# Performance work log

Hardware: AMD Instinct MI355X
Metric: run time of the kernel (lower is better)

The kernel has to match this reference:

```python
import jax, jax.numpy as jnp
import numpy as np

N_HEAD = 16
N_FEAT = 1024
D_K = N_FEAT // N_HEAD


def setup_inputs() -> dict:
    key = jax.random.key(0)
    ks = jax.random.split(key, 12)
    B, T, F = 4, 2048, N_FEAT
    s = 1.0 / np.sqrt(F)
    return {
        "query": jax.random.normal(ks[0], (B, T, F), dtype=jnp.float32),
        "key": jax.random.normal(ks[1], (B, T, F), dtype=jnp.float32),
        "value": jax.random.normal(ks[2], (B, T, F), dtype=jnp.float32),
        "mask": jnp.ones((B, 1, T), dtype=jnp.int32),
        "Wq": jax.random.normal(ks[3], (F, F), dtype=jnp.float32) * s,
        "bq": jax.random.normal(ks[4], (F,), dtype=jnp.float32) * 0.01,
        "Wk": jax.random.normal(ks[5], (F, F), dtype=jnp.float32) * s,
        "bk": jax.random.normal(ks[6], (F,), dtype=jnp.float32) * 0.01,
        "Wv": jax.random.normal(ks[7], (F, F), dtype=jnp.float32) * s,
        "bv": jax.random.normal(ks[8], (F,), dtype=jnp.float32) * 0.01,
        "Wo": jax.random.normal(ks[9], (F, F), dtype=jnp.float32) * s,
        "bo": jax.random.normal(ks[10], (F,), dtype=jnp.float32) * 0.01,
    }


def reference(query, key, value, mask, Wq, bq, Wk, bk, Wv, bv, Wo, bo):
    B, Tq, F = query.shape
    Tk = key.shape[1]
    h, dk = N_HEAD, D_K
    # torch nn.Linear: y = x @ W.T + b ; then view [B,T,h,dk] and transpose to [B,h,T,dk]
    q = (query @ Wq.T + bq).reshape(B, Tq, h, dk).transpose(0, 2, 1, 3)
    k = (key @ Wk.T + bk).reshape(B, Tk, h, dk).transpose(0, 2, 1, 3)
    v = (value @ Wv.T + bv).reshape(B, Tk, h, dk).transpose(0, 2, 1, 3)
    scale = 1.0 / np.sqrt(dk).astype(np.float32)
    scores = jnp.einsum("bhqd,bhkd->bhqk", q, k) * scale  # [B,h,Tq,Tk]
    # mask [B,1,Tk] -> unsqueeze(1) -> [B,1,1,Tk], True where mask == 0 (padded)
    pad = (mask[:, None, :, :] == 0)
    min_value = jnp.finfo(scores.dtype).min
    scores = jnp.where(pad, min_value, scores)
    atten = jax.nn.softmax(scores, axis=-1)
    atten = jnp.where(pad, 0.0, atten)
    # dropout_rate = 0.0 (eval): identity
    x = jnp.einsum("bhqk,bhkd->bhqd", atten, v)  # [B,h,Tq,dk]
    x = x.transpose(0, 2, 1, 3).reshape(B, Tq, h * dk)
    return x @ Wo.T + bo
```

## Files before the change

kernel.cpp:

```cpp
#include <hip/hip_runtime.h>
#include <hip/hip_bf16.h>


typedef unsigned short u16;
typedef unsigned long long u64;
typedef __attribute__((ext_vector_type(8))) short short8;
typedef __attribute__((ext_vector_type(4))) float f32x4;
typedef __attribute__((ext_vector_type(16))) float f32x16;
typedef __attribute__((ext_vector_type(4))) unsigned int u32x4;

#define GLOAD16(g, l) __builtin_amdgcn_global_load_lds( \
    (const __attribute__((address_space(1))) unsigned int*)(g), \
    (__attribute__((address_space(3))) unsigned int*)(l), 16, 0, 0)

__device__ __forceinline__ u16 f2bf(float x) {
  unsigned int u = __float_as_uint(x);
  return (u16)((u + 0x7fffu + ((u >> 16) & 1u)) >> 16);
}

__device__ __forceinline__ float fexp2(float x) {
#if __has_builtin(__builtin_amdgcn_exp2f)
  return __builtin_amdgcn_exp2f(x);
#else
  return exp2f(x);
#endif
}

__device__ __forceinline__ unsigned cvtpk(float lo, float hi) {
  unsigned r;
  asm("v_cvt_pk_bf16_f32 %0, %1, %2" : "=v"(r) : "v"(lo), "v"(hi));
  return r;
}

struct CvtArgs {
  const float* src[4];
  u16* dst[4];
};

__global__ __launch_bounds__(256) void cvt_multi(CvtArgs a, int shift) {
  const int id = blockIdx.x * 256 + threadIdx.x;
  const int seg = id >> shift;
  const int off = id & ((1 << shift) - 1);
  float4 v = ((const float4*)a.src[seg])[off];
  ushort4 o;
  o.x = f2bf(v.x); o.y = f2bf(v.y); o.z = f2bf(v.z); o.w = f2bf(v.w);
  ((ushort4*)a.dst[seg])[off] = o;
}

template <int EPI>
__global__ __launch_bounds__(256) void gemm_bt(const u16* __restrict__ A,
                                               const u16* __restrict__ Bw,
                                               const float* __restrict__ bias,
                                               void* __restrict__ Cout,
                                               float scale) {
  __shared__ u16 As[128 * 64];
  __shared__ u16 Bs[128 * 64];
  const int t = threadIdx.x;
  const int lane = t & 63;
  const int w = t >> 6;
  const int wm = w >> 1, wn = w & 1;
  const int l15 = lane & 15, l4 = lane >> 4;

  const int bid = blockIdx.x;
  const int swz = (bid & 7) * 64 + (bid >> 3);
  const int brow = swz >> 3;
  const int bcol = swz & 7;

  f32x4 acc[4][4] = {};

  const int srow = t >> 3;
  const int sbyte = (t & 7) * 16;

  for (int kt = 0; kt < 16; ++kt) {
    const int k0 = kt * 64;
    __syncthreads();
#pragma unroll
    for (int i = 0; i < 4; ++i) {
      const int r = i * 32 + srow;
      const int sb = sbyte ^ ((r & 7) << 4);
      GLOAD16((const char*)(A + (size_t)(brow * 128 + r) * 1024 + k0) + sb,
              &As[(i * 4096 + t * 16) >> 1]);
      GLOAD16((const char*)(Bw + (size_t)(bcol * 128 + r) * 1024 + k0) + sb,
              &Bs[(i * 4096 + t * 16) >> 1]);
    }
    __syncthreads();
#pragma unroll
    for (int kf = 0; kf < 2; ++kf) {
      short8 af[4], bfv[4];
#pragma unroll
      for (int mi = 0; mi < 4; ++mi) {
        const int r = wm * 64 + mi * 16 + l15;
        const int byt = r * 128 + ((kf * 64 + l4 * 16) ^ ((r & 7) << 4));
        af[mi] = *(const short8*)&As[byt >> 1];
      }
#pragma unroll
      for (int ni = 0; ni < 4; ++ni) {
        const int r = wn * 64 + ni * 16 + l15;
        const int byt = r * 128 + ((kf * 64 + l4 * 16) ^ ((r & 7) << 4));
        bfv[ni] = *(const short8*)&Bs[byt >> 1];
      }
#pragma unroll
      for (int mi = 0; mi < 4; ++mi)
#pragma unroll
        for (int ni = 0; ni < 4; ++ni)
          acc[mi][ni] = __builtin_amdgcn_mfma_f32_16x16x32_bf16(
              af[mi], bfv[ni], acc[mi][ni], 0, 0, 0);
    }
  }

#pragma unroll
  for (int ni = 0; ni < 4; ++ni) {
    const int n = bcol * 128 + wn * 64 + ni * 16 + l15;
    const float bn = bias[n];
#pragma unroll
    for (int mi = 0; mi < 4; ++mi) {
      const int mb = brow * 128 + wm * 64 + mi * 16 + l4 * 4;
#pragma unroll
      for (int r = 0; r < 4; ++r) {
        const float v = acc[mi][ni][r] + bn;
        const int m = mb + r;
        const int b_ = m >> 11, tok = m & 2047, h_ = n >> 6, d = n & 63;
        if (EPI == 0) {
          ((u16*)Cout)[(((size_t)(b_ * 16 + h_) * 2048 + tok) << 6) + d] = f2bf(v * scale);
        } else if (EPI == 2) {
          ((u16*)Cout)[(((size_t)(b_ * 16 + h_) * 64 + d) << 11) + tok] = f2bf(v);
        } else {
          ((float*)Cout)[(size_t)m * 1024 + n] = v;
        }
      }
    }
  }
}

__global__ __launch_bounds__(256, 2) void attn_fwd5(const u16* __restrict__ Q,
                                                    const u16* __restrict__ Kp,
                                                    const u16* __restrict__ Vt,
                                                    const int* __restrict__ mask,
                                                    u16* __restrict__ ctx) {
  __shared__ u16 Ks[2][64 * 64];
  __shared__ u16 Vs[2][64 * 64];

  const int t = threadIdx.x, lane = t & 63, w = t >> 6;
  const int q31 = lane & 31, hi = lane >> 5;

  const int bid = blockIdx.x;
  const int swz = (bid & 7) * 64 + (bid >> 3);
  const int bh = swz >> 3;
  const int b_ = bh >> 4, h_ = bh & 15;
  const int q0 = (swz & 7) * 256 + w * 64;
  const size_t headO = (size_t)bh * 131072;

  short8 qfA[4], qfB[4];
  {
    const u16* qrowA = Q + headO + (size_t)(q0 + q31) * 64 + hi * 8;
    const u16* qrowB = qrowA + 32 * 64;
#pragma unroll
    for (int ds = 0; ds < 4; ++ds) {
      qfA[ds] = *(const short8*)(qrowA + ds * 16);
      qfB[ds] = *(const short8*)(qrowB + ds * 16);
    }
  }

  const int srow = t >> 3;
  const int sbyte = (t & 7) * 16;

#define STAGE_KV(bufi, kb)                                                      \
  {                                                                             \
    _Pragma("unroll") for (int i = 0; i < 2; ++i) {                             \
      const int r = i * 32 + srow;                                              \
      const int sb = sbyte ^ ((r & 7) << 4);                                    \
      GLOAD16((const char*)(Kp + headO + (size_t)((kb) + r) * 64) + sb,         \
              &Ks[bufi][(i * 4096 + t * 16) >> 1]);                             \
      GLOAD16((const char*)(Vt + headO + (size_t)r * 2048 + (kb)) + sb,         \
              &Vs[bufi][(i * 4096 + t * 16) >> 1]);                             \
    }                                                                           \
  }

#define PACK(sv, pfa, pfb)                                                      \
  {                                                                             \
    const unsigned w0 = cvtpk(sv[0], sv[1]),   w1 = cvtpk(sv[2], sv[3]);        \
    const unsigned w2 = cvtpk(sv[4], sv[5]),   w3 = cvtpk(sv[6], sv[7]);        \
    const unsigned w4 = cvtpk(sv[8], sv[9]),   w5 = cvtpk(sv[10], sv[11]);      \
    const unsigned w6 = cvtpk(sv[12], sv[13]), w7 = cvtpk(sv[14], sv[15]);      \
    const unsigned x0 = (unsigned)__shfl_xor((int)(hi ? w0 : w2), 32);          \
    const unsigned x1 = (unsigned)__shfl_xor((int)(hi ? w1 : w3), 32);          \
    const unsigned y0 = (unsigned)__shfl_xor((int)(hi ? w4 : w6), 32);          \
    const unsigned y1 = (unsigned)__shfl_xor((int)(hi ? w5 : w7), 32);          \
    u32x4 fa = hi ? (u32x4){x0, x1, w2, w3} : (u32x4){w0, w1, x0, x1};          \
    u32x4 fb = hi ? (u32x4){y0, y1, w6, w7} : (u32x4){w4, w5, y0, y1};          \
    pfa = __builtin_bit_cast(short8, fa);                                       \
    pfb = __builtin_bit_cast(short8, fb);                                       \
  }

  f32x16 oA0 = {}, oA1 = {}, oB0 = {}, oB1 = {};
  float lA = 0.f, lB = 0.f;
  const int kcol = hi * 16;
  const int rswz = (q31 & 7) << 4;

  STAGE_KV(0, 0);
  int mk = mask[b_ * 2048 + lane];
  __syncthreads();

  int buf = 0;
  for (int kt = 0; kt < 32; ++kt) {
    const int kb = kt * 64;
    if (kt + 1 < 32) STAGE_KV(buf ^ 1, kb + 64);
    const int mk_next = (kt + 1 < 32) ? mask[b_ * 2048 + kb + 64 + lane] : 0;
    const u64 bits = __ballot(mk != 0);

#pragma unroll
    for (int half = 0; half < 2; ++half) {
      f32x16 sA = {}, sB = {};
      __builtin_amdgcn_s_setprio(1);
#pragma unroll
      for (int ds = 0; ds < 4; ++ds) {
        const int byt = (half * 32 + q31) * 128 + ((ds * 32 + kcol) ^ rswz);
        short8 ka = *(const short8*)&Ks[buf][byt >> 1];
        sA = __builtin_amdgcn_mfma_f32_32x32x16_bf16(ka, qfA[ds], sA, 0, 0, 0);
        sB = __builtin_amdgcn_mfma_f32_32x32x16_bf16(ka, qfB[ds], sB, 0, 0, 0);
      }
      __builtin_amdgcn_s_setprio(0);

      if (bits == ~0ull) {
#pragma unroll
        for (int r = 0; r < 16; ++r) { sA[r] = fexp2(sA[r]); sB[r] = fexp2(sB[r]); }
      } else {
#pragma unroll
        for (int r = 0; r < 16; ++r) {
          const int k0 = half * 32 + (r & 3) + 8 * (r >> 2) + 4 * hi;
          const bool on = (bits >> k0) & 1;
          sA[r] = on ? fexp2(sA[r]) : 0.f;
          sB[r] = on ? fexp2(sB[r]) : 0.f;
        }
      }

      {
        float a0 = 0.f, a1 = 0.f, b0 = 0.f, b1 = 0.f;
#pragma unroll
        for (int r = 0; r < 16; r += 2) {
          a0 += sA[r]; a1 += sA[r + 1];
          b0 += sB[r]; b1 += sB[r + 1];
        }
        lA += a0 + a1;
        lB += b0 + b1;
      }

      short8 pA0, pA1, pB0, pB1;
      PACK(sA, pA0, pA1);
      PACK(sB, pB0, pB1);

      __builtin_amdgcn_s_setprio(1);
      {
        const int rb0 = q31 * 128, rb1 = (32 + q31) * 128;
        const int c0 = (half * 64 + kcol) ^ rswz;
        const int c1 = (half * 64 + 32 + kcol) ^ rswz;
        short8 va;
        va = *(const short8*)&Vs[buf][(rb0 + c0) >> 1];
        oA0 = __builtin_amdgcn_mfma_f32_32x32x16_bf16(va, pA0, oA0, 0, 0, 0);
        oB0 = __builtin_amdgcn_mfma_f32_32x32x16_bf16(va, pB0, oB0, 0, 0, 0);
        va = *(const short8*)&Vs[buf][(rb0 + c1) >> 1];
        oA0 = __builtin_amdgcn_mfma_f32_32x32x16_bf16(va, pA1, oA0, 0, 0, 0);
        oB0 = __builtin_amdgcn_mfma_f32_32x32x16_bf16(va, pB1, oB0, 0, 0, 0);
        va = *(const short8*)&Vs[buf][(rb1 + c0) >> 1];
        oA1 = __builtin_amdgcn_mfma_f32_32x32x16_bf16(va, pA0, oA1, 0, 0, 0);
        oB1 = __builtin_amdgcn_mfma_f32_32x32x16_bf16(va, pB0, oB1, 0, 0, 0);
        va = *(const short8*)&Vs[buf][(rb1 + c1) >> 1];
        oA1 = __builtin_amdgcn_mfma_f32_32x32x16_bf16(va, pA1, oA1, 0, 0, 0);
        oB1 = __builtin_amdgcn_mfma_f32_32x32x16_bf16(va, pB1, oB1, 0, 0, 0);
      }
      __builtin_amdgcn_s_setprio(0);
    }

    mk = mk_next;
    __syncthreads();
    buf ^= 1;
  }
#undef STAGE_KV

  lA += __shfl_xor(lA, 32);
  lB += __shfl_xor(lB, 32);
  const float invA = lA > 0.f ? 1.f / lA : 0.f;
  const float invB = lB > 0.f ? 1.f / lB : 0.f;
  const int tokA = q0 + q31;
  u16* crowA = ctx + ((size_t)b_ * 2048 + tokA) * 1024 + h_ * 64 + 4 * hi;
  u16* crowB = crowA + 32 * 1024;
#pragma unroll
  for (int g = 0; g < 4; ++g) {
    unsigned u0, u1;
    u0 = cvtpk(oA0[4 * g + 0] * invA, oA0[4 * g + 1] * invA);
    u1 = cvtpk(oA0[4 * g + 2] * invA, oA0[4 * g + 3] * invA);
    *(uint2*)(crowA + 8 * g) = make_uint2(u0, u1);
    u0 = cvtpk(oA1[4 * g + 0] * invA, oA1[4 * g + 1] * invA);
    u1 = cvtpk(oA1[4 * g + 2] * invA, oA1[4 * g + 3] * invA);
    *(uint2*)(crowA + 32 + 8 * g) = make_uint2(u0, u1);
    u0 = cvtpk(oB0[4 * g + 0] * invB, oB0[4 * g + 1] * invB);
    u1 = cvtpk(oB0[4 * g + 2] * invB, oB0[4 * g + 3] * invB);
    *(uint2*)(crowB + 8 * g) = make_uint2(u0, u1);
    u0 = cvtpk(oB1[4 * g + 0] * invB, oB1[4 * g + 1] * invB);
    u1 = cvtpk(oB1[4 * g + 2] * invB, oB1[4 * g + 3] * invB);
    *(uint2*)(crowB + 32 + 8 * g) = make_uint2(u0, u1);
  }
}

extern "C" void kernel_launch(void* const* d_in, const int* in_sizes, int n_in,
                              void* d_out, int out_size, void* d_ws, size_t ws_size,
                              hipStream_t stream) {
  const float* q_in = (const float*)d_in[0];
  const float* k_in = (const float*)d_in[1];
  const float* v_in = (const float*)d_in[2];
  const int*   mask = (const int*)d_in[3];
  const float* Wq = (const float*)d_in[4];
  const float* bq = (const float*)d_in[5];
  const float* Wk = (const float*)d_in[6];
  const float* bk = (const float*)d_in[7];
  const float* Wv = (const float*)d_in[8];
  const float* bv = (const float*)d_in[9];
  const float* Wo = (const float*)d_in[10];
  const float* bo = (const float*)d_in[11];
  float* out = (float*)d_out;

  char* ws = (char*)d_ws;
  u16* xq = (u16*)(ws);
  u16* xk = (u16*)(ws + 16777216);
  u16* xv = (u16*)(ws + 33554432);
  u16* Qp = (u16*)(ws + 50331648);
  u16* Kp = (u16*)(ws + 67108864);
  u16* Vtb = (u16*)(ws + 83886080);
  u16* wqb = (u16*)(ws + 100663296);
  u16* wkb = (u16*)(ws + 102760448);
  u16* wvb = (u16*)(ws + 104857600);
  u16* wob = (u16*)(ws + 106954752);
  u16* ctx = xk;

  CvtArgs big;
  big.src[0] = q_in; big.src[1] = k_in; big.src[2] = v_in; big.src[3] = v_in;
  big.dst[0] = xq;   big.dst[1] = xk;   big.dst[2] = xv;   big.dst[3] = xv;
  cvt_multi<<<3 * 8192, 256, 0, stream>>>(big, 21);
  CvtArgs wts;
  wts.src[0] = Wq;  wts.src[1] = Wk;  wts.src[2] = Wv;  wts.src[3] = Wo;
  wts.dst[0] = wqb; wts.dst[1] = wkb; wts.dst[2] = wvb; wts.dst[3] = wob;
  cvt_multi<<<4 * 1024, 256, 0, stream>>>(wts, 18);

  const float C_SCALE = 0.18033688011112042f;
  gemm_bt<0><<<512, 256, 0, stream>>>(xq, wqb, bq, Qp, C_SCALE);
  gemm_bt<0><<<512, 256, 0, stream>>>(xk, wkb, bk, Kp, 1.0f);
  gemm_bt<2><<<512, 256, 0, stream>>>(xv, wvb, bv, Vtb, 1.0f);

  attn_fwd5<<<512, 256, 0, stream>>>(Qp, Kp, Vtb, mask, ctx);

  gemm_bt<1><<<512, 256, 0, stream>>>(ctx, wob, bo, out, 1.0f);
}
```

Baseline: 227.5 us.

## Fuse fp32-to-bf16 activation conversion into batched double-buffered QKV GEMM

Drops the separate fp32-to-bf16 pass over the query/key/value activations. A single 1536-block QKV GEMM now loads fp32 A tiles into registers and converts them to bf16 while writing LDS. Both GEMMs gain double-buffered LDS with prefetch of the next k-tile, plus s_setprio around the MFMAs. The Q/K/V epilogue now stages results in LDS so global stores are coalesced 16-byte writes. This saves a full activation read/write round trip and several launches, at the cost of doubling fp32 A load traffic per tile and using 64KB LDS per block.

```diff
diff --git a/kernel.cpp b/kernel.cpp
--- a/kernel.cpp
+++ b/kernel.cpp
@@ -47,17 +47,173 @@
   ((ushort4*)a.dst[seg])[off] = o;
 }
 
-template <int EPI>
-__global__ __launch_bounds__(256) void gemm_bt(const u16* __restrict__ A,
-                                               const u16* __restrict__ Bw,
-                                               const float* __restrict__ bias,
-                                               void* __restrict__ Cout,
-                                               float scale) {
-  __shared__ u16 As[128 * 64];
-  __shared__ u16 Bs[128 * 64];
-  const int t = threadIdx.x;
-  const int lane = t & 63;
-  const int w = t >> 6;
+struct QKVArgs {
+  const float* A[3];
+  const u16* W[3];
+  const float* bias[3];
+  u16* out[3];
+};
+
+__global__ __launch_bounds__(256, 2) void qkv_gemm(QKVArgs args) {
+  __shared__ __align__(16) char smem[65536];
+
+  const int t = threadIdx.x, lane = t & 63, w = t >> 6;
+  const int wm = w >> 1, wn = w & 1;
+  const int l15 = lane & 15, l4 = lane >> 4;
+
+  const int bid = blockIdx.x;
+  const int seg = bid >> 9;
+  const int inner = bid & 511;
+  const int swz = (inner & 7) * 64 + (inner >> 3);
+  const int brow = swz >> 3;
+  const int bcol = swz & 7;
+
+  const float* Ag = args.A[seg];
+  const u16* Wg = args.W[seg];
+  const float* bias = args.bias[seg];
+  u16* outp = args.out[seg];
+  const float scale = (seg == 0) ? 0.18033688011112042f : 1.0f;
+
+  const int arow = t >> 1;
+  const int as0 = (t & 1) * 4;
+  const int srow = t >> 3;
+  const int sbyte = (t & 7) * 16;
+
+  f32x4 acc[4][4] = {};
+  float4 areg[8];
+
+#define ALOAD(k0)                                                                \
+  {                                                                              \
+    const float4* p = (const float4*)(Ag + (size_t)(brow * 128 + arow) * 1024 +  \
+                                      (k0) + as0 * 8);                           \
+    _Pragma("unroll") for (int j = 0; j < 8; ++j) areg[j] = p[j];                \
+  }
+#define AWRITE(bufptr)                                                           \
+  {                                                                              \
+    _Pragma("unroll") for (int i = 0; i < 4; ++i) {                              \
+      u32x4 pk = {cvtpk(areg[2 * i].x, areg[2 * i].y),                           \
+                  cvtpk(areg[2 * i].z, areg[2 * i].w),                           \
+                  cvtpk(areg[2 * i + 1].x, areg[2 * i + 1].y),                   \
+                  cvtpk(areg[2 * i + 1].z, areg[2 * i + 1].w)};                  \
+      *(u32x4*)((char*)(bufptr) + arow * 128 +                                   \
+                (((as0 + i) * 16) ^ ((arow & 7) << 4))) = pk;                    \
+    }                                                                            \
+  }
+#define STAGEB(bufptr, Bsrc, colbase, k0)                                        \
+  {                                                                              \
+    _Pragma("unroll") for (int i = 0; i < 4; ++i) {                              \
+      const int r = i * 32 + srow;                                               \
+      const int sb = sbyte ^ ((r & 7) << 4);                                     \
+      GLOAD16((const char*)(Bsrc + (size_t)((colbase) + r) * 1024 + (k0)) + sb,  \
+              (char*)(bufptr) + i * 4096 + t * 16);                              \
+    }                                                                            \
+  }
+
+  ALOAD(0);
+  STAGEB(smem + 32768, Wg, bcol * 128, 0);
+  AWRITE(smem);
+  __syncthreads();
+
+  int buf = 0;
+  for (int kt = 0; kt < 16; ++kt) {
+    if (kt < 15) {
+      ALOAD(kt * 64 + 64);
+      STAGEB(smem + 32768 + ((buf ^ 1) << 14), Wg, bcol * 128, kt * 64 + 64);
+    }
+    const char* Ab = smem + (buf << 14);
+    const char* Bb = smem + 32768 + (buf << 14);
+#pragma unroll
+    for (int kf = 0; kf < 2; ++kf) {
+      short8 af[4], bfv[4];
+#pragma unroll
+      for (int mi = 0; mi < 4; ++mi) {
+        const int r = wm * 64 + mi * 16 + l15;
+        af[mi] = *(const short8*)(Ab + r * 128 + ((kf * 64 + l4 * 16) ^ ((r & 7) << 4)));
+      }
+#pragma unroll
+      for (int ni = 0; ni < 4; ++ni) {
+        const int r = wn * 64 + ni * 16 + l15;
+        bfv[ni] = *(const short8*)(Bb + r * 128 + ((kf * 64 + l4 * 16) ^ ((r & 7) << 4)));
+      }
+      __builtin_amdgcn_s_setprio(1);
+#pragma unroll
+      for (int mi = 0; mi < 4; ++mi)
+#pragma unroll
+        for (int ni = 0; ni < 4; ++ni)
+          acc[mi][ni] = __builtin_amdgcn_mfma_f32_16x16x32_bf16(
+              af[mi], bfv[ni], acc[mi][ni], 0, 0, 0);
+      __builtin_amdgcn_s_setprio(0);
+    }
+    if (kt < 15) AWRITE(smem + ((buf ^ 1) << 14));
+    __syncthreads();
+    buf ^= 1;
+  }
+#undef ALOAD
+#undef AWRITE
+
+  u16* cb = (u16*)smem;
+  const int bglob = brow >> 4;
+  const int tokbase = (brow & 15) * 128;
+
+  if (seg < 2) {
+#pragma unroll
+    for (int ni = 0; ni < 4; ++ni) {
+      const int n = wn * 64 + ni * 16 + l15;
+      const float b = bias[bcol * 128 + n];
+#pragma unroll
+      for (int mi = 0; mi < 4; ++mi) {
+        const int m0 = wm * 64 + mi * 16 + l4 * 4;
+#pragma unroll
+        for (int r = 0; r < 4; ++r)
+          cb[(m0 + r) * 136 + n] = f2bf((acc[mi][ni][r] + b) * scale);
+      }
+    }
+    __syncthreads();
+#pragma unroll
+    for (int j = 0; j < 8; ++j) {
+      const int c = t + 256 * j;
+      const int m = c >> 4, nc = c & 15;
+      u32x4 v = *(const u32x4*)(cb + m * 136 + nc * 8);
+      const int ng = bcol * 128 + nc * 8;
+      const int h = ng >> 6, d0 = ng & 63;
+      *(u32x4*)(outp + (((size_t)(bglob * 16 + h) * 2048 + tokbase + m) << 6) + d0) = v;
+    }
+  } else {
+#pragma unroll
+    for (int ni = 0; ni < 4; ++ni) {
+      const int n = wn * 64 + ni * 16 + l15;
+      const float b = bias[bcol * 128 + n];
+#pragma unroll
+      for (int mi = 0; mi < 4; ++mi) {
+        const int m0 = wm * 64 + mi * 16 + l4 * 4;
+        ushort4 pk4;
+        pk4.x = f2bf(acc[mi][ni][0] + b);
+        pk4.y = f2bf(acc[mi][ni][1] + b);
+        pk4.z = f2bf(acc[mi][ni][2] + b);
+        pk4.w = f2bf(acc[mi][ni][3] + b);
+        *(ushort4*)(cb + n * 136 + m0) = pk4;
+      }
+    }
+    __syncthreads();
+#pragma unroll
+    for (int j = 0; j < 8; ++j) {
+      const int c = t + 256 * j;
+      const int n = c >> 4, mc = c & 15;
+      u32x4 v = *(const u32x4*)(cb + n * 136 + mc * 8);
+      const int ng = bcol * 128 + n;
+      const int h = ng >> 6, d = ng & 63;
+      *(u32x4*)(outp + (((size_t)(bglob * 16 + h) * 64 + d) << 11) + tokbase + mc * 8) = v;
+    }
+  }
+}
+
+__global__ __launch_bounds__(256, 2) void out_gemm(const u16* __restrict__ A,
+                                                   const u16* __restrict__ Wg,
+                                                   const float* __restrict__ bias,
+                                                   float* __restrict__ outp) {
+  __shared__ __align__(16) char smem[65536];
+
+  const int t = threadIdx.x, lane = t & 63, w = t >> 6;
   const int wm = w >> 1, wn = w & 1;
   const int l15 = lane & 15, l4 = lane >> 4;
 
@@ -66,47 +222,49 @@
   const int brow = swz >> 3;
   const int bcol = swz & 7;
 
-  f32x4 acc[4][4] = {};
-
   const int srow = t >> 3;
   const int sbyte = (t & 7) * 16;
 
+  f32x4 acc[4][4] = {};
+
+  STAGEB(smem, A, brow * 128, 0);
+  STAGEB(smem + 32768, Wg, bcol * 128, 0);
+  __syncthreads();
+
+  int buf = 0;
   for (int kt = 0; kt < 16; ++kt) {
-    const int k0 = kt * 64;
-    __syncthreads();
-#pragma unroll
-    for (int i = 0; i < 4; ++i) {
-      const int r = i * 32 + srow;
-      const int sb = sbyte ^ ((r & 7) << 4);
-      GLOAD16((const char*)(A + (size_t)(brow * 128 + r) * 1024 + k0) + sb,
-              &As[(i * 4096 + t * 16) >> 1]);
-      GLOAD16((const char*)(Bw + (size_t)(bcol * 128 + r) * 1024 + k0) + sb,
-              &Bs[(i * 4096 + t * 16) >> 1]);
-    }
-    __syncthreads();
+    if (kt < 15) {
+      STAGEB(smem + ((buf ^ 1) << 14), A, brow * 128, kt * 64 + 64);
+      STAGEB(smem + 32768 + ((buf ^ 1) << 14), Wg, bcol * 128, kt * 64 + 64);
+    }
+    const char* Ab = smem + (buf << 14);
+    const char* Bb = smem + 32768 + (buf << 14);
 #pragma unroll
     for (int kf = 0; kf < 2; ++kf) {
       short8 af[4], bfv[4];
 #pragma unroll
       for (int mi = 0; mi < 4; ++mi) {
         const int r = wm * 64 + mi * 16 + l15;
-        const int byt = r * 128 + ((kf * 64 + l4 * 16) ^ ((r & 7) << 4));
-        af[mi] = *(const short8*)&As[byt >> 1];
+        af[mi] = *(const short8*)(Ab + r * 128 + ((kf * 64 + l4 * 16) ^ ((r & 7) << 4)));
       }
 #pragma unroll
       for (int ni = 0; ni < 4; ++ni) {
         const int r = wn * 64 + ni * 16 + l15;
-        const int byt = r * 128 + ((kf * 64 + l4 * 16) ^ ((r & 7) << 4));
-        bfv[ni] = *(const short8*)&Bs[byt >> 1];
-      }
+        bfv[ni] = *(const short8*)(Bb + r * 128 + ((kf * 64 + l4 * 16) ^ ((r & 7) << 4)));
+      }
+      __builtin_amdgcn_s_setprio(1);
 #pragma unroll
       for (int mi = 0; mi < 4; ++mi)
 #pragma unroll
         for (int ni = 0; ni < 4; ++ni)
           acc[mi][ni] = __builtin_amdgcn_mfma_f32_16x16x32_bf16(
               af[mi], bfv[ni], acc[mi][ni], 0, 0, 0);
-    }
-  }
+      __builtin_amdgcn_s_setprio(0);
+    }
+    __syncthreads();
+    buf ^= 1;
+  }
+#undef STAGEB
 
 #pragma unroll
   for (int ni = 0; ni < 4; ++ni) {
@@ -116,18 +274,8 @@
     for (int mi = 0; mi < 4; ++mi) {
       const int mb = brow * 128 + wm * 64 + mi * 16 + l4 * 4;
 #pragma unroll
-      for (int r = 0; r < 4; ++r) {
-        const float v = acc[mi][ni][r] + bn;
-        const int m = mb + r;
-        const int b_ = m >> 11, tok = m & 2047, h_ = n >> 6, d = n & 63;
-        if (EPI == 0) {
-          ((u16*)Cout)[(((size_t)(b_ * 16 + h_) * 2048 + tok) << 6) + d] = f2bf(v * scale);
-        } else if (EPI == 2) {
-          ((u16*)Cout)[(((size_t)(b_ * 16 + h_) * 64 + d) << 11) + tok] = f2bf(v);
-        } else {
-          ((float*)Cout)[(size_t)m * 1024 + n] = v;
-        }
-      }
+      for (int r = 0; r < 4; ++r)
+        outp[(size_t)(mb + r) * 1024 + n] = acc[mi][ni][r] + bn;
     }
   }
 }
@@ -320,9 +468,7 @@
   float* out = (float*)d_out;
 
   char* ws = (char*)d_ws;
-  u16* xq = (u16*)(ws);
-  u16* xk = (u16*)(ws + 16777216);
-  u16* xv = (u16*)(ws + 33554432);
+  u16* ctx = (u16*)(ws);
   u16* Qp = (u16*)(ws + 50331648);
   u16* Kp = (u16*)(ws + 67108864);
   u16* Vtb = (u16*)(ws + 83886080);
@@ -330,23 +476,20 @@
   u16* wkb = (u16*)(ws + 102760448);
   u16* wvb = (u16*)(ws + 104857600);
   u16* wob = (u16*)(ws + 106954752);
-  u16* ctx = xk;
-
-  CvtArgs big;
-  big.src[0] = q_in; big.src[1] = k_in; big.src[2] = v_in; big.src[3] = v_in;
-  big.dst[0] = xq;   big.dst[1] = xk;   big.dst[2] = xv;   big.dst[3] = xv;
-  cvt_multi<<<3 * 8192, 256, 0, stream>>>(big, 21);
+
   CvtArgs wts;
   wts.src[0] = Wq;  wts.src[1] = Wk;  wts.src[2] = Wv;  wts.src[3] = Wo;
   wts.dst[0] = wqb; wts.dst[1] = wkb; wts.dst[2] = wvb; wts.dst[3] = wob;
   cvt_multi<<<4 * 1024, 256, 0, stream>>>(wts, 18);
 
-  const float C_SCALE = 0.18033688011112042f;
-  gemm_bt<0><<<512, 256, 0, stream>>>(xq, wqb, bq, Qp, C_SCALE);
-  gemm_bt<0><<<512, 256, 0, stream>>>(xk, wkb, bk, Kp, 1.0f);
-  gemm_bt<2><<<512, 256, 0, stream>>>(xv, wvb, bv, Vtb, 1.0f);
+  QKVArgs qa;
+  qa.A[0] = q_in; qa.A[1] = k_in; qa.A[2] = v_in;
+  qa.W[0] = wqb;  qa.W[1] = wkb;  qa.W[2] = wvb;
+  qa.bias[0] = bq; qa.bias[1] = bk; qa.bias[2] = bv;
+  qa.out[0] = Qp;  qa.out[1] = Kp;  qa.out[2] = Vtb;
+  qkv_gemm<<<1536, 256, 0, stream>>>(qa);
 
   attn_fwd5<<<512, 256, 0, stream>>>(Qp, Kp, Vtb, mask, ctx);
 
-  gemm_bt<1><<<512, 256, 0, stream>>>(ctx, wob, bo, out, 1.0f);
-}
+  out_gemm<<<512, 256, 0, stream>>>(ctx, wob, bo, out);
+}
```

After: 257.9 us. 1.13x slower.
